# Kernel optimization log

Measured on AMD Instinct MI355X. Metric: run time of the kernel, lower is better.

## Reference

```python
import jax, jax.numpy as jnp
import numpy as np

W, L, D = 4096, 32, 256
WORD_VOCAB, CHR_VOCAB = 50000, 128


def conv1d(x, w, b):
    # x: [N, C_in, T], w: [C_out, C_in, 3], padding=1 (same)
    y = jax.lax.conv_general_dilated(
        x, w, window_strides=(1,), padding=[(1, 1)],
        dimension_numbers=("NCW", "OIW", "NCW"))
    return y + b[None, :, None]


def setup_inputs() -> dict:
    key = jax.random.key(0)
    ks = jax.random.split(key, 12)
    words = jax.random.randint(ks[0], (W,), 0, WORD_VOCAB, dtype=jnp.int32)
    words_in_char = jax.random.randint(ks[1], (W, L), 0, CHR_VOCAB, dtype=jnp.int32)
    s = 0.02
    word_emb = (jax.random.normal(ks[2], (WORD_VOCAB, D), jnp.float32) * s).at[0].set(0.0)  # padding_idx=0
    chr_emb = (jax.random.normal(ks[3], (CHR_VOCAB, D), jnp.float32) * s).at[0].set(0.0)
    conv_chr_w = jax.random.normal(ks[4], (D, D, 3), jnp.float32) * s
    conv_chr_b = jax.random.normal(ks[5], (D,), jnp.float32) * s
    conv_sent_w = jax.random.normal(ks[6], (2 * D, 2 * D, 3), jnp.float32) * s
    conv_sent_b = jax.random.normal(ks[7], (2 * D,), jnp.float32) * s
    w1 = jax.random.normal(ks[8], (4 * D, 2 * D), jnp.float32) * s
    b1 = jax.random.normal(ks[9], (4 * D,), jnp.float32) * s
    w2 = jax.random.normal(ks[10], (2, 4 * D), jnp.float32) * s
    b2 = jax.random.normal(ks[11], (2,), jnp.float32) * s
    return dict(words=words, words_in_char=words_in_char,
                word_emb=word_emb, chr_emb=chr_emb,
                conv_chr_w=conv_chr_w, conv_chr_b=conv_chr_b,
                conv_sent_w=conv_sent_w, conv_sent_b=conv_sent_b,
                w1=w1, b1=b1, w2=w2, b2=b2)


def reference(words, words_in_char, word_emb, chr_emb,
              conv_chr_w, conv_chr_b, conv_sent_w, conv_sent_b,
              w1, b1, w2, b2):
    # word embeddings: [W, D]
    vector_wrds = word_emb[words]
    # char path, batched over all words (equivalent to the per-word loop):
    ch = chr_emb[words_in_char]                      # [W, L, D]
    ch = jnp.transpose(ch, (0, 2, 1))                # [W, D, L]
    wc = conv1d(ch, conv_chr_w, conv_chr_b)          # [W, D, L]
    vector_wchs = jnp.max(wc, axis=2)                # [W, D]
    # sentence conv over the word axis
    u = jnp.concatenate([vector_wrds, vector_wchs], axis=1)  # [W, 2D]
    u = u.T[None, :, :]                              # [1, 2D, W]
    r = conv1d(u, conv_sent_w, conv_sent_b)          # [1, 2D, W]
    r = jnp.max(r, axis=2)                           # [1, 2D]
    h = jnp.tanh(r @ w1.T + b1)                      # [1, 4D]
    return h @ w2.T + b2                             # [1, 2]
```

## Files before the change

### kernel.cpp

```cpp
#include <hip/hip_runtime.h>
#include <hip/hip_bf16.h>
#include <math.h>

#define NW 4096
#define NL 32
#define ND 256
#define ND2 512

typedef __attribute__((ext_vector_type(8))) short short8;
typedef __attribute__((ext_vector_type(4))) float floatx4;

__device__ inline float bitsf(unsigned u) {
  union { unsigned u; float f; } v;
  v.u = u;
  return v.f;
}


__global__ __launch_bounds__(256) void prep_kernel(
    const float* __restrict__ conv_sent_w, const float* __restrict__ conv_chr_w,
    float* __restrict__ wT, __hip_bfloat16* __restrict__ Wb,
    short* __restrict__ u_base, int* __restrict__ ctr) {
  int b = blockIdx.x;
  int tid = threadIdx.x;
  if (b < 3072) {
    int idx = b * 256 + tid;
    float v = conv_sent_w[idx];
    int co = idx / 1536;
    int rem = idx - co * 1536;
    int ci = rem / 3;
    int k = rem - ci * 3;
    Wb[k * 262144 + co * 512 + ci] = __float2bfloat16(v);
  } else if (b < 3840) {
    int idx = (b - 3072) * 256 + tid;
    float v = conv_chr_w[idx];
    int co = idx / 768;
    int rem = idx - co * 768;
    int ci = rem / 3;
    int k = rem - ci * 3;
    wT[k * 65536 + ci * 256 + co] = v;
  } else {
    u_base[tid] = 0;
    u_base[tid + 256] = 0;
    u_base[4097 * 512 + tid] = 0;
    u_base[4097 * 512 + tid + 256] = 0;
    if (tid == 0) ctr[0] = 0;
  }
}

__global__ __launch_bounds__(256) void table_kernel(
    const float* __restrict__ chr_emb, const float* __restrict__ wT,
    __hip_bfloat16* __restrict__ Tb) {
  __shared__ float s_e[4][256];
  int k = blockIdx.x >> 5;
  int c0 = (blockIdx.x & 31) * 4;
  int co = threadIdx.x;
#pragma unroll
  for (int j = 0; j < 4; ++j) s_e[j][co] = chr_emb[(c0 + j) * 256 + co];
  __syncthreads();
  const float* wk = wT + k * 65536;
  float a0 = 0.f, a1 = 0.f, a2 = 0.f, a3 = 0.f;
#pragma unroll 8
  for (int ci = 0; ci < 256; ++ci) {
    float w = wk[ci * 256 + co];
    a0 = fmaf(s_e[0][ci], w, a0);
    a1 = fmaf(s_e[1][ci], w, a1);
    a2 = fmaf(s_e[2][ci], w, a2);
    a3 = fmaf(s_e[3][ci], w, a3);
  }
  int base = ((co >> 6) * 3 + k) * 8192 + (co & 63);
  Tb[base + (c0 + 0) * 64] = __float2bfloat16(a0);
  Tb[base + (c0 + 1) * 64] = __float2bfloat16(a1);
  Tb[base + (c0 + 2) * 64] = __float2bfloat16(a2);
  Tb[base + (c0 + 3) * 64] = __float2bfloat16(a3);
}

__global__ __launch_bounds__(256) void char_word_kernel(
    const int* __restrict__ words, const int* __restrict__ wic,
    const __hip_bfloat16* __restrict__ Tb, const float* __restrict__ word_emb,
    const float* __restrict__ bias, __hip_bfloat16* __restrict__ u0) {
  __shared__ short sT[3 * 128 * 64];
  __shared__ int s_wic[32 * 32];
  __shared__ int s_wid[32];
  const int ct = blockIdx.x >> 7;
  const int w0 = (blockIdx.x & 127) * 32;
  const int tid = threadIdx.x;
  {
    const uint4* src = (const uint4*)((const short*)Tb + ct * 24576);
    uint4* dst = (uint4*)sT;
#pragma unroll
    for (int i = 0; i < 12; ++i) dst[tid + i * 256] = src[tid + i * 256];
    ((int4*)s_wic)[tid] = ((const int4*)(wic + w0 * 32))[tid];
    if (tid < 32) s_wid[tid] = words[w0 + tid];
  }
  __syncthreads();
  {
    const int co_l = tid & 63, slot = tid >> 6;
#pragma unroll
    for (int wi = 0; wi < 8; ++wi) {
      int wl = slot * 8 + wi;
      u0[(w0 + wl) * ND2 + ct * 64 + co_l] =
          __float2bfloat16(word_emb[s_wid[wl] * ND + ct * 64 + co_l]);
    }
  }
  const int wave = tid >> 6, lane = tid & 63;
  const int half = lane >> 5, co2 = (lane & 31) * 2;
  const float2 bb = *(const float2*)&bias[ct * 64 + co2];
  const short* T0p = sT;
  const short* T1p = sT + 8192;
  const short* T2p = sT + 16384;
#pragma unroll
  for (int p = 0; p < 4; ++p) {
    const int wl = wave * 8 + p * 2 + half;
    int chv[32];
    const int4* c4 = (const int4*)(s_wic + wl * 32);
#pragma unroll
    for (int j = 0; j < 8; ++j) {
      int4 cc = c4[j];
      chv[4 * j + 0] = cc.x; chv[4 * j + 1] = cc.y;
      chv[4 * j + 2] = cc.z; chv[4 * j + 3] = cc.w;
    }
    float m0 = -INFINITY, m1 = -INFINITY;
#pragma unroll
    for (int t = 0; t < NL; ++t) {
      unsigned v1 = *(const unsigned*)&T1p[chv[t] * 64 + co2];
      float s0 = bitsf(v1 << 16);
      float s1 = bitsf(v1 & 0xffff0000u);
      if (t > 0) {
        unsigned v0 = *(const unsigned*)&T0p[chv[t - 1] * 64 + co2];
        s0 += bitsf(v0 << 16);
        s1 += bitsf(v0 & 0xffff0000u);
      }
      if (t < NL - 1) {
        unsigned v2 = *(const unsigned*)&T2p[chv[t + 1] * 64 + co2];
        s0 += bitsf(v2 << 16);
        s1 += bitsf(v2 & 0xffff0000u);
      }
      m0 = fmaxf(m0, s0);
      m1 = fmaxf(m1, s1);
    }
    __hip_bfloat162 hh;
    hh.x = __float2bfloat16(m0 + bb.x);
    hh.y = __float2bfloat16(m1 + bb.y);
    *(__hip_bfloat162*)&u0[(w0 + wl) * ND2 + ND + ct * 64 + co2] = hh;
  }
}

__global__ __launch_bounds__(256, 2) void sent_conv_mfma(
    const __hip_bfloat16* __restrict__ u0,
    const __hip_bfloat16* __restrict__ Wb,
    float* __restrict__ partial) {
  __shared__ short As[64 * 64];
  __shared__ short Bs[64 * 64];
  __shared__ float sm[4][32];
  const int tid = threadIdx.x;
  const int t0 = blockIdx.x * 64;
  const int co0 = blockIdx.y * 64;
  const int wave = tid >> 6, lane = tid & 63;
  const int wy = wave >> 1, wx = wave & 1;
  const int m = lane & 15, q = lane >> 4;

  floatx4 acc[2][2];
#pragma unroll
  for (int i = 0; i < 2; ++i)
#pragma unroll
    for (int j = 0; j < 2; ++j) acc[i][j] = (floatx4){0.f, 0.f, 0.f, 0.f};

  int aoff[2][2], boff[2][2];
#pragma unroll
  for (int kk = 0; kk < 2; ++kk) {
#pragma unroll
    for (int i = 0; i < 2; ++i) {
      int row = wy * 32 + i * 16 + m;
      aoff[kk][i] = row * 64 + (((kk * 4 + q) ^ (row & 7)) * 8);
      row = wx * 32 + i * 16 + m;
      boff[kk][i] = row * 64 + (((kk * 4 + q) ^ (row & 7)) * 8);
    }
  }

  const int sc = tid & 7, sr = tid >> 3;
  const int swc = (sc ^ (sr & 7)) * 8;
  const short* WbS = (const short*)Wb;
  const short* uS = (const short*)u0;

  for (int s = 0; s < 24; ++s) {
    int k = s >> 3, ci0 = (s & 7) << 6;
    const short* WbK = WbS + k * 262144 + (co0 + sr) * 512 + ci0 + sc * 8;
    const short* uK = uS + (t0 + sr + k - 1) * 512 + ci0 + sc * 8;
    uint4 a0 = *(const uint4*)(WbK);
    uint4 a1 = *(const uint4*)(WbK + 32 * 512);
    uint4 b0 = *(const uint4*)(uK);
    uint4 b1 = *(const uint4*)(uK + 32 * 512);
    *(uint4*)&As[sr * 64 + swc] = a0;
    *(uint4*)&As[(sr + 32) * 64 + swc] = a1;
    *(uint4*)&Bs[sr * 64 + swc] = b0;
    *(uint4*)&Bs[(sr + 32) * 64 + swc] = b1;
    __syncthreads();
#pragma unroll
    for (int kk = 0; kk < 2; ++kk) {
      short8 av0 = *(const short8*)&As[aoff[kk][0]];
      short8 av1 = *(const short8*)&As[aoff[kk][1]];
      short8 bv0 = *(const short8*)&Bs[boff[kk][0]];
      short8 bv1 = *(const short8*)&Bs[boff[kk][1]];
      acc[0][0] = __builtin_amdgcn_mfma_f32_16x16x32_bf16(av0, bv0, acc[0][0], 0, 0, 0);
      acc[0][1] = __builtin_amdgcn_mfma_f32_16x16x32_bf16(av0, bv1, acc[0][1], 0, 0, 0);
      acc[1][0] = __builtin_amdgcn_mfma_f32_16x16x32_bf16(av1, bv0, acc[1][0], 0, 0, 0);
      acc[1][1] = __builtin_amdgcn_mfma_f32_16x16x32_bf16(av1, bv1, acc[1][1], 0, 0, 0);
    }
    __syncthreads();
  }

#pragma unroll
  for (int i = 0; i < 2; ++i)
#pragma unroll
    for (int r = 0; r < 4; ++r) {
      float x = fmaxf(acc[i][0][r], acc[i][1][r]);
#pragma unroll
      for (int off = 1; off < 16; off <<= 1)
        x = fmaxf(x, __shfl_xor(x, off, 64));
      if (m == 0) sm[wave][i * 16 + q * 4 + r] = x;
    }
  __syncthreads();
  if (tid < 64) {
    int whalf = tid >> 5;
    float v = fmaxf(sm[whalf * 2 + 0][tid & 31], sm[whalf * 2 + 1][tid & 31]);
    partial[(co0 + tid) * 64 + blockIdx.x] = v;
  }
}

__global__ __launch_bounds__(512) void fc12_kernel(
    const float* __restrict__ partial, const float* __restrict__ bs,
    const float* __restrict__ w1, const float* __restrict__ b1,
    const float* __restrict__ w2, const float* __restrict__ b2,
    float* __restrict__ h, int* __restrict__ ctr, float* __restrict__ out) {
  __shared__ float s_r[512];
  __shared__ int s_last;
  int tid = threadIdx.x;
  {
    const float4* p = (const float4*)(partial + tid * 64);
    float mm = -INFINITY;
#pragma unroll
    for (int j = 0; j < 16; ++j) {
      float4 v = p[j];
      mm = fmaxf(mm, fmaxf(fmaxf(v.x, v.y), fmaxf(v.z, v.w)));
    }
    s_r[tid] = mm + bs[tid];
  }
  __syncthreads();
  int wave = tid >> 6, lane = tid & 63;
  int o = blockIdx.x * 8 + wave;
  const float4* wv = (const float4*)(w1 + o * 512 + lane * 8);
  const float4* rv = (const float4*)(s_r + lane * 8);
  float4 w0 = wv[0], w1v = wv[1];
  float4 r0 = rv[0], r1 = rv[1];
  float acc = w0.x * r0.x + w0.y * r0.y + w0.z * r0.z + w0.w * r0.w +
              w1v.x * r1.x + w1v.y * r1.y + w1v.z * r1.z + w1v.w * r1.w;
#pragma unroll
  for (int off = 32; off >= 1; off >>= 1) acc += __shfl_down(acc, off, 64);
  if (lane == 0) h[o] = tanhf(acc + b1[o]);
  __syncthreads();
  if (tid == 0) {
    int old = __hip_atomic_fetch_add(ctr, 1, __ATOMIC_RELEASE,
                                     __HIP_MEMORY_SCOPE_AGENT);
    s_last = (old == 127) ? 1 : 0;
  }
  __syncthreads();
  if (s_last) {
    __builtin_amdgcn_fence(__ATOMIC_ACQUIRE, "agent");
    if (tid < 128) {
      int o2 = tid >> 6;
      int lane2 = tid & 63;
      float acc2 = 0.f;
#pragma unroll
      for (int j = 0; j < 16; ++j)
        acc2 = fmaf(w2[o2 * 1024 + lane2 + j * 64], h[lane2 + j * 64], acc2);
#pragma unroll
      for (int off = 32; off >= 1; off >>= 1) acc2 += __shfl_down(acc2, off, 64);
      if (lane2 == 0) out[o2] = acc2 + b2[o2];
    }
  }
}

extern "C" void kernel_launch(void* const* d_in, const int* in_sizes, int n_in,
                              void* d_out, int out_size, void* d_ws, size_t ws_size,
                              hipStream_t stream) {
  const int*   words       = (const int*)d_in[0];
  const int*   wic         = (const int*)d_in[1];
  const float* word_emb    = (const float*)d_in[2];
  const float* chr_emb     = (const float*)d_in[3];
  const float* conv_chr_w  = (const float*)d_in[4];
  const float* conv_chr_b  = (const float*)d_in[5];
  const float* conv_sent_w = (const float*)d_in[6];
  const float* conv_sent_b = (const float*)d_in[7];
  const float* w1          = (const float*)d_in[8];
  const float* b1          = (const float*)d_in[9];
  const float* w2          = (const float*)d_in[10];
  const float* b2          = (const float*)d_in[11];
  float* out = (float*)d_out;

  float* ws    = (float*)d_ws;
  float* wT    = ws;
  float* part  = wT + 196608;
  float* h_buf = part + 32768;
  int*   ctr   = (int*)(h_buf + 1024);
  short* Tb    = (short*)(ctr + 4);
  short* u_base = Tb + 98304;
  __hip_bfloat16* u0 = (__hip_bfloat16*)(u_base + 512);
  __hip_bfloat16* Wb = (__hip_bfloat16*)(u_base + 4098 * 512);

  prep_kernel<<<3841, 256, 0, stream>>>(conv_sent_w, conv_chr_w, wT, Wb,
                                        u_base, ctr);
  table_kernel<<<96, 256, 0, stream>>>(chr_emb, wT, (__hip_bfloat16*)Tb);
  char_word_kernel<<<512, 256, 0, stream>>>(words, wic, (const __hip_bfloat16*)Tb,
                                            word_emb, conv_chr_b, u0);
  sent_conv_mfma<<<dim3(64, 8), 256, 0, stream>>>(u0, Wb, part);
  fc12_kernel<<<128, 512, 0, stream>>>(part, conv_sent_b, w1, b1, w2, b2,
                                       h_buf, ctr, out);
}
```

Before: 158.1 us.

## Fuse prep and table kernels via atomic counter; double-buffer sentence conv LDS

Merges the weight-transpose prep and the char table build into one launch. Table blocks spin on an agent-scope atomic counter until all conv_chr_w transpose blocks have finished, so one kernel launch boundary goes away. The counter is now cleared with a memset, and fc12 uses a separate counter slot. Separately, the sentence conv MFMA loop now double-buffers its LDS tiles, prefetching the next stage's global loads into registers while computing the current one, which halves the barriers per stage. The spin-wait risks deadlock if the table blocks get scheduled before the producer blocks can run, and the double buffer raises LDS and register use.

```diff
diff --git a/kernel.cpp b/kernel.cpp
--- a/kernel.cpp
+++ b/kernel.cpp
@@ -17,62 +17,72 @@
 }
 
 
-__global__ __launch_bounds__(256) void prep_kernel(
+__global__ __launch_bounds__(256) void prep_table_kernel(
     const float* __restrict__ conv_sent_w, const float* __restrict__ conv_chr_w,
-    float* __restrict__ wT, __hip_bfloat16* __restrict__ Wb,
-    short* __restrict__ u_base, int* __restrict__ ctr) {
-  int b = blockIdx.x;
-  int tid = threadIdx.x;
-  if (b < 3072) {
+    const float* __restrict__ chr_emb, float* __restrict__ wT,
+    __hip_bfloat16* __restrict__ Wb, __hip_bfloat16* __restrict__ Tb,
+    short* __restrict__ u_base, int* __restrict__ ctrA) {
+  __shared__ float s_e[4][256];
+  const int b = blockIdx.x;
+  const int tid = threadIdx.x;
+  if (b < 768) {
     int idx = b * 256 + tid;
+    float v = conv_chr_w[idx];
+    int co = idx / 768;
+    int rem = idx - co * 768;
+    int ci = rem / 3;
+    int k = rem - ci * 3;
+    wT[k * 65536 + ci * 256 + co] = v;
+    __syncthreads();
+    if (tid == 0)
+      __hip_atomic_fetch_add(ctrA, 1, __ATOMIC_RELEASE, __HIP_MEMORY_SCOPE_AGENT);
+    return;
+  }
+  if (b < 864) {
+    if (tid == 0) {
+      while (__hip_atomic_load(ctrA, __ATOMIC_RELAXED, __HIP_MEMORY_SCOPE_AGENT) < 768)
+        __builtin_amdgcn_s_sleep(2);
+    }
+    __syncthreads();
+    __builtin_amdgcn_fence(__ATOMIC_ACQUIRE, "agent");
+    const int tb = b - 768;
+    const int k = tb >> 5;
+    const int c0 = (tb & 31) * 4;
+    const int co = tid;
+#pragma unroll
+    for (int j = 0; j < 4; ++j) s_e[j][co] = chr_emb[(c0 + j) * 256 + co];
+    __syncthreads();
+    const float* wk = wT + k * 65536;
+    float a0 = 0.f, a1 = 0.f, a2 = 0.f, a3 = 0.f;
+#pragma unroll 8
+    for (int ci = 0; ci < 256; ++ci) {
+      float w = wk[ci * 256 + co];
+      a0 = fmaf(s_e[0][ci], w, a0);
+      a1 = fmaf(s_e[1][ci], w, a1);
+      a2 = fmaf(s_e[2][ci], w, a2);
+      a3 = fmaf(s_e[3][ci], w, a3);
+    }
+    int base = ((co >> 6) * 3 + k) * 8192 + (co & 63);
+    Tb[base + (c0 + 0) * 64] = __float2bfloat16(a0);
+    Tb[base + (c0 + 1) * 64] = __float2bfloat16(a1);
+    Tb[base + (c0 + 2) * 64] = __float2bfloat16(a2);
+    Tb[base + (c0 + 3) * 64] = __float2bfloat16(a3);
+    return;
+  }
+  if (b < 3936) {
+    int idx = (b - 864) * 256 + tid;
     float v = conv_sent_w[idx];
     int co = idx / 1536;
     int rem = idx - co * 1536;
     int ci = rem / 3;
     int k = rem - ci * 3;
     Wb[k * 262144 + co * 512 + ci] = __float2bfloat16(v);
-  } else if (b < 3840) {
-    int idx = (b - 3072) * 256 + tid;
-    float v = conv_chr_w[idx];
-    int co = idx / 768;
-    int rem = idx - co * 768;
-    int ci = rem / 3;
-    int k = rem - ci * 3;
-    wT[k * 65536 + ci * 256 + co] = v;
-  } else {
-    u_base[tid] = 0;
-    u_base[tid + 256] = 0;
-    u_base[4097 * 512 + tid] = 0;
-    u_base[4097 * 512 + tid + 256] = 0;
-    if (tid == 0) ctr[0] = 0;
-  }
-}
-
-__global__ __launch_bounds__(256) void table_kernel(
-    const float* __restrict__ chr_emb, const float* __restrict__ wT,
-    __hip_bfloat16* __restrict__ Tb) {
-  __shared__ float s_e[4][256];
-  int k = blockIdx.x >> 5;
-  int c0 = (blockIdx.x & 31) * 4;
-  int co = threadIdx.x;
-#pragma unroll
-  for (int j = 0; j < 4; ++j) s_e[j][co] = chr_emb[(c0 + j) * 256 + co];
-  __syncthreads();
-  const float* wk = wT + k * 65536;
-  float a0 = 0.f, a1 = 0.f, a2 = 0.f, a3 = 0.f;
-#pragma unroll 8
-  for (int ci = 0; ci < 256; ++ci) {
-    float w = wk[ci * 256 + co];
-    a0 = fmaf(s_e[0][ci], w, a0);
-    a1 = fmaf(s_e[1][ci], w, a1);
-    a2 = fmaf(s_e[2][ci], w, a2);
-    a3 = fmaf(s_e[3][ci], w, a3);
-  }
-  int base = ((co >> 6) * 3 + k) * 8192 + (co & 63);
-  Tb[base + (c0 + 0) * 64] = __float2bfloat16(a0);
-  Tb[base + (c0 + 1) * 64] = __float2bfloat16(a1);
-  Tb[base + (c0 + 2) * 64] = __float2bfloat16(a2);
-  Tb[base + (c0 + 3) * 64] = __float2bfloat16(a3);
+    return;
+  }
+  u_base[tid] = 0;
+  u_base[tid + 256] = 0;
+  u_base[4097 * 512 + tid] = 0;
+  u_base[4097 * 512 + tid + 256] = 0;
 }
 
 __global__ __launch_bounds__(256) void char_word_kernel(
@@ -150,8 +160,8 @@
     const __hip_bfloat16* __restrict__ u0,
     const __hip_bfloat16* __restrict__ Wb,
     float* __restrict__ partial) {
-  __shared__ short As[64 * 64];
-  __shared__ short Bs[64 * 64];
+  __shared__ short As[2][64 * 64];
+  __shared__ short Bs[2][64 * 64];
   __shared__ float sm[4][32];
   const int tid = threadIdx.x;
   const int t0 = blockIdx.x * 64;
@@ -183,32 +193,46 @@
   const short* WbS = (const short*)Wb;
   const short* uS = (const short*)u0;
 
-  for (int s = 0; s < 24; ++s) {
-    int k = s >> 3, ci0 = (s & 7) << 6;
+  uint4 ra0, ra1, rb0, rb1;
+  auto LOADS = [&](int s2) {
+    int k = s2 >> 3, ci0 = (s2 & 7) << 6;
     const short* WbK = WbS + k * 262144 + (co0 + sr) * 512 + ci0 + sc * 8;
     const short* uK = uS + (t0 + sr + k - 1) * 512 + ci0 + sc * 8;
-    uint4 a0 = *(const uint4*)(WbK);
-    uint4 a1 = *(const uint4*)(WbK + 32 * 512);
-    uint4 b0 = *(const uint4*)(uK);
-    uint4 b1 = *(const uint4*)(uK + 32 * 512);
-    *(uint4*)&As[sr * 64 + swc] = a0;
-    *(uint4*)&As[(sr + 32) * 64 + swc] = a1;
-    *(uint4*)&Bs[sr * 64 + swc] = b0;
-    *(uint4*)&Bs[(sr + 32) * 64 + swc] = b1;
-    __syncthreads();
+    ra0 = *(const uint4*)(WbK);
+    ra1 = *(const uint4*)(WbK + 32 * 512);
+    rb0 = *(const uint4*)(uK);
+    rb1 = *(const uint4*)(uK + 32 * 512);
+  };
+  auto WRITE = [&](int buf) {
+    *(uint4*)&As[buf][sr * 64 + swc] = ra0;
+    *(uint4*)&As[buf][(sr + 32) * 64 + swc] = ra1;
+    *(uint4*)&Bs[buf][sr * 64 + swc] = rb0;
+    *(uint4*)&Bs[buf][(sr + 32) * 64 + swc] = rb1;
+  };
+  auto MFMA = [&](int buf) {
 #pragma unroll
     for (int kk = 0; kk < 2; ++kk) {
-      short8 av0 = *(const short8*)&As[aoff[kk][0]];
-      short8 av1 = *(const short8*)&As[aoff[kk][1]];
-      short8 bv0 = *(const short8*)&Bs[boff[kk][0]];
-      short8 bv1 = *(const short8*)&Bs[boff[kk][1]];
+      short8 av0 = *(const short8*)&As[buf][aoff[kk][0]];
+      short8 av1 = *(const short8*)&As[buf][aoff[kk][1]];
+      short8 bv0 = *(const short8*)&Bs[buf][boff[kk][0]];
+      short8 bv1 = *(const short8*)&Bs[buf][boff[kk][1]];
       acc[0][0] = __builtin_amdgcn_mfma_f32_16x16x32_bf16(av0, bv0, acc[0][0], 0, 0, 0);
       acc[0][1] = __builtin_amdgcn_mfma_f32_16x16x32_bf16(av0, bv1, acc[0][1], 0, 0, 0);
       acc[1][0] = __builtin_amdgcn_mfma_f32_16x16x32_bf16(av1, bv0, acc[1][0], 0, 0, 0);
       acc[1][1] = __builtin_amdgcn_mfma_f32_16x16x32_bf16(av1, bv1, acc[1][1], 0, 0, 0);
     }
+  };
+
+  LOADS(0);
+  WRITE(0);
+  __syncthreads();
+  for (int s = 0; s < 23; ++s) {
+    LOADS(s + 1);
+    MFMA(s & 1);
+    WRITE((s + 1) & 1);
     __syncthreads();
   }
+  MFMA(23 & 1);
 
 #pragma unroll
   for (int i = 0; i < 2; ++i)
@@ -299,21 +323,22 @@
   float* out = (float*)d_out;
 
   float* ws    = (float*)d_ws;
-  float* wT    = ws;
+  int*   ctr   = (int*)ws;
+  float* wT    = ws + 8;
   float* part  = wT + 196608;
   float* h_buf = part + 32768;
-  int*   ctr   = (int*)(h_buf + 1024);
-  short* Tb    = (short*)(ctr + 4);
+  short* Tb    = (short*)(h_buf + 1024);
   short* u_base = Tb + 98304;
   __hip_bfloat16* u0 = (__hip_bfloat16*)(u_base + 512);
   __hip_bfloat16* Wb = (__hip_bfloat16*)(u_base + 4098 * 512);
 
-  prep_kernel<<<3841, 256, 0, stream>>>(conv_sent_w, conv_chr_w, wT, Wb,
-                                        u_base, ctr);
-  table_kernel<<<96, 256, 0, stream>>>(chr_emb, wT, (__hip_bfloat16*)Tb);
+  hipMemsetAsync(ctr, 0, 32, stream);
+  prep_table_kernel<<<3937, 256, 0, stream>>>(conv_sent_w, conv_chr_w, chr_emb,
+                                              wT, Wb, (__hip_bfloat16*)Tb,
+                                              u_base, ctr);
   char_word_kernel<<<512, 256, 0, stream>>>(words, wic, (const __hip_bfloat16*)Tb,
                                             word_emb, conv_chr_b, u0);
   sent_conv_mfma<<<dim3(64, 8), 256, 0, stream>>>(u0, Wb, part);
   fc12_kernel<<<128, 512, 0, stream>>>(part, conv_sent_b, w1, b1, w2, b2,
-                                       h_buf, ctr, out);
-}
+                                       h_buf, ctr + 4, out);
+}
```

Measured after the change: 197.9 us. 1.25x slower.

## Double-buffer LDS tiles in sentence conv MFMA and coalesce weight prep writes

Applied to the files above, without the earlier changes.

The sentence-conv MFMA kernel now uses two LDS buffers and prefetches the next K-slice into registers while the MFMAs run on the current one. This cuts the per-iteration syncs from two to one and overlaps global load latency with compute. The prep kernel now indexes by output position, so bf16 weight writes are coalesced and the reads become strided. LDS use doubles, which may affect the 2-blocks-per-CU occupancy target.

```diff
diff --git a/kernel.cpp b/kernel.cpp
--- a/kernel.cpp
+++ b/kernel.cpp
@@ -25,12 +25,11 @@
   int tid = threadIdx.x;
   if (b < 3072) {
     int idx = b * 256 + tid;
-    float v = conv_sent_w[idx];
-    int co = idx / 1536;
-    int rem = idx - co * 1536;
-    int ci = rem / 3;
-    int k = rem - ci * 3;
-    Wb[k * 262144 + co * 512 + ci] = __float2bfloat16(v);
+    int k = idx >> 18;
+    int rem = idx & 262143;
+    int co = rem >> 9;
+    int ci = rem & 511;
+    Wb[idx] = __float2bfloat16(conv_sent_w[co * 1536 + ci * 3 + k]);
   } else if (b < 3840) {
     int idx = (b - 3072) * 256 + tid;
     float v = conv_chr_w[idx];
@@ -150,8 +149,8 @@
     const __hip_bfloat16* __restrict__ u0,
     const __hip_bfloat16* __restrict__ Wb,
     float* __restrict__ partial) {
-  __shared__ short As[64 * 64];
-  __shared__ short Bs[64 * 64];
+  __shared__ short As[2][64 * 64];
+  __shared__ short Bs[2][64 * 64];
   __shared__ float sm[4][32];
   const int tid = threadIdx.x;
   const int t0 = blockIdx.x * 64;
@@ -183,32 +182,46 @@
   const short* WbS = (const short*)Wb;
   const short* uS = (const short*)u0;
 
-  for (int s = 0; s < 24; ++s) {
-    int k = s >> 3, ci0 = (s & 7) << 6;
+  uint4 ra0, ra1, rb0, rb1;
+  auto LOADS = [&](int s2) {
+    int k = s2 >> 3, ci0 = (s2 & 7) << 6;
     const short* WbK = WbS + k * 262144 + (co0 + sr) * 512 + ci0 + sc * 8;
     const short* uK = uS + (t0 + sr + k - 1) * 512 + ci0 + sc * 8;
-    uint4 a0 = *(const uint4*)(WbK);
-    uint4 a1 = *(const uint4*)(WbK + 32 * 512);
-    uint4 b0 = *(const uint4*)(uK);
-    uint4 b1 = *(const uint4*)(uK + 32 * 512);
-    *(uint4*)&As[sr * 64 + swc] = a0;
-    *(uint4*)&As[(sr + 32) * 64 + swc] = a1;
-    *(uint4*)&Bs[sr * 64 + swc] = b0;
-    *(uint4*)&Bs[(sr + 32) * 64 + swc] = b1;
-    __syncthreads();
+    ra0 = *(const uint4*)(WbK);
+    ra1 = *(const uint4*)(WbK + 32 * 512);
+    rb0 = *(const uint4*)(uK);
+    rb1 = *(const uint4*)(uK + 32 * 512);
+  };
+  auto WRITE = [&](int buf) {
+    *(uint4*)&As[buf][sr * 64 + swc] = ra0;
+    *(uint4*)&As[buf][(sr + 32) * 64 + swc] = ra1;
+    *(uint4*)&Bs[buf][sr * 64 + swc] = rb0;
+    *(uint4*)&Bs[buf][(sr + 32) * 64 + swc] = rb1;
+  };
+  auto MFMA = [&](int buf) {
 #pragma unroll
     for (int kk = 0; kk < 2; ++kk) {
-      short8 av0 = *(const short8*)&As[aoff[kk][0]];
-      short8 av1 = *(const short8*)&As[aoff[kk][1]];
-      short8 bv0 = *(const short8*)&Bs[boff[kk][0]];
-      short8 bv1 = *(const short8*)&Bs[boff[kk][1]];
+      short8 av0 = *(const short8*)&As[buf][aoff[kk][0]];
+      short8 av1 = *(const short8*)&As[buf][aoff[kk][1]];
+      short8 bv0 = *(const short8*)&Bs[buf][boff[kk][0]];
+      short8 bv1 = *(const short8*)&Bs[buf][boff[kk][1]];
       acc[0][0] = __builtin_amdgcn_mfma_f32_16x16x32_bf16(av0, bv0, acc[0][0], 0, 0, 0);
       acc[0][1] = __builtin_amdgcn_mfma_f32_16x16x32_bf16(av0, bv1, acc[0][1], 0, 0, 0);
       acc[1][0] = __builtin_amdgcn_mfma_f32_16x16x32_bf16(av1, bv0, acc[1][0], 0, 0, 0);
       acc[1][1] = __builtin_amdgcn_mfma_f32_16x16x32_bf16(av1, bv1, acc[1][1], 0, 0, 0);
     }
+  };
+
+  LOADS(0);
+  WRITE(0);
+  __syncthreads();
+  for (int s = 0; s < 23; ++s) {
+    LOADS(s + 1);
+    MFMA(s & 1);
+    WRITE((s + 1) & 1);
     __syncthreads();
   }
+  MFMA(23 & 1);
 
 #pragma unroll
   for (int i = 0; i < 2; ++i)
```

Result: no change. 155.2 us (-1.9%).

## Load sentence-conv MFMA operands straight from global memory, drop LDS staging

Applied to the files above, without the earlier changes.

The sentence conv MFMA kernel no longer stages A/B tiles through shared memory with barriers. Each wave now loads its bf16 fragments directly from global memory (relying on L1/L2 for reuse), and occupancy is raised to 4 blocks per SM. The prep kernel also turns the weight transpose into a gather, so its bf16 writes are coalesced. This trades LDS traffic and syncs for redundant global and cache loads, with less data reuse per wave.

```diff
diff --git a/kernel.cpp b/kernel.cpp
--- a/kernel.cpp
+++ b/kernel.cpp
@@ -25,12 +25,11 @@
   int tid = threadIdx.x;
   if (b < 3072) {
     int idx = b * 256 + tid;
-    float v = conv_sent_w[idx];
-    int co = idx / 1536;
-    int rem = idx - co * 1536;
-    int ci = rem / 3;
-    int k = rem - ci * 3;
-    Wb[k * 262144 + co * 512 + ci] = __float2bfloat16(v);
+    int k = idx >> 18;
+    int rem = idx & 262143;
+    int co = rem >> 9;
+    int ci = rem & 511;
+    Wb[idx] = __float2bfloat16(conv_sent_w[co * 1536 + ci * 3 + k]);
   } else if (b < 3840) {
     int idx = (b - 3072) * 256 + tid;
     float v = conv_chr_w[idx];
@@ -146,12 +145,10 @@
   }
 }
 
-__global__ __launch_bounds__(256, 2) void sent_conv_mfma(
+__global__ __launch_bounds__(256, 4) void sent_conv_mfma(
     const __hip_bfloat16* __restrict__ u0,
     const __hip_bfloat16* __restrict__ Wb,
     float* __restrict__ partial) {
-  __shared__ short As[64 * 64];
-  __shared__ short Bs[64 * 64];
   __shared__ float sm[4][32];
   const int tid = threadIdx.x;
   const int t0 = blockIdx.x * 64;
@@ -166,48 +163,30 @@
 #pragma unroll
     for (int j = 0; j < 2; ++j) acc[i][j] = (floatx4){0.f, 0.f, 0.f, 0.f};
 
-  int aoff[2][2], boff[2][2];
-#pragma unroll
-  for (int kk = 0; kk < 2; ++kk) {
-#pragma unroll
-    for (int i = 0; i < 2; ++i) {
-      int row = wy * 32 + i * 16 + m;
-      aoff[kk][i] = row * 64 + (((kk * 4 + q) ^ (row & 7)) * 8);
-      row = wx * 32 + i * 16 + m;
-      boff[kk][i] = row * 64 + (((kk * 4 + q) ^ (row & 7)) * 8);
-    }
-  }
-
-  const int sc = tid & 7, sr = tid >> 3;
-  const int swc = (sc ^ (sr & 7)) * 8;
   const short* WbS = (const short*)Wb;
   const short* uS = (const short*)u0;
-
+  const short* A0 = WbS + (co0 + wy * 32 + m) * 512 + q * 8;
+  const short* A1 = A0 + 16 * 512;
+  const short* B0 = uS + (t0 + wx * 32 + m - 1) * 512 + q * 8;
+  const short* B1 = B0 + 16 * 512;
+
+#pragma unroll 2
   for (int s = 0; s < 24; ++s) {
-    int k = s >> 3, ci0 = (s & 7) << 6;
-    const short* WbK = WbS + k * 262144 + (co0 + sr) * 512 + ci0 + sc * 8;
-    const short* uK = uS + (t0 + sr + k - 1) * 512 + ci0 + sc * 8;
-    uint4 a0 = *(const uint4*)(WbK);
-    uint4 a1 = *(const uint4*)(WbK + 32 * 512);
-    uint4 b0 = *(const uint4*)(uK);
-    uint4 b1 = *(const uint4*)(uK + 32 * 512);
-    *(uint4*)&As[sr * 64 + swc] = a0;
-    *(uint4*)&As[(sr + 32) * 64 + swc] = a1;
-    *(uint4*)&Bs[sr * 64 + swc] = b0;
-    *(uint4*)&Bs[(sr + 32) * 64 + swc] = b1;
-    __syncthreads();
+    const int k = s >> 3, ci0 = (s & 7) << 6;
+    const int ao = k * 262144 + ci0;
+    const int bo = k * 512 + ci0;
 #pragma unroll
     for (int kk = 0; kk < 2; ++kk) {
-      short8 av0 = *(const short8*)&As[aoff[kk][0]];
-      short8 av1 = *(const short8*)&As[aoff[kk][1]];
-      short8 bv0 = *(const short8*)&Bs[boff[kk][0]];
-      short8 bv1 = *(const short8*)&Bs[boff[kk][1]];
+      const int off = kk * 32;
+      short8 av0 = *(const short8*)(A0 + ao + off);
+      short8 av1 = *(const short8*)(A1 + ao + off);
+      short8 bv0 = *(const short8*)(B0 + bo + off);
+      short8 bv1 = *(const short8*)(B1 + bo + off);
       acc[0][0] = __builtin_amdgcn_mfma_f32_16x16x32_bf16(av0, bv0, acc[0][0], 0, 0, 0);
       acc[0][1] = __builtin_amdgcn_mfma_f32_16x16x32_bf16(av0, bv1, acc[0][1], 0, 0, 0);
       acc[1][0] = __builtin_amdgcn_mfma_f32_16x16x32_bf16(av1, bv0, acc[1][0], 0, 0, 0);
       acc[1][1] = __builtin_amdgcn_mfma_f32_16x16x32_bf16(av1, bv1, acc[1][1], 0, 0, 0);
     }
-    __syncthreads();
   }
 
 #pragma unroll
```

Measured after the change: 186.2 us. 1.18x slower.
